# Optimization experiments

Hardware: AMD Instinct MI355X
Metric: run time of the kernel (lower is better)

## Reference

```python
import jax, jax.numpy as jnp
import numpy as np

N = 100000
G = 65          # grid points per axis
C = 16          # channels per receptor grid
IN_FEATS = 16
LIG_F = 128
REC_F = 128
BOTH_F = 128
HID = 256
POCKET_RADIUS = 16.0

# standard uniform cubic B-spline basis matrix (rows: powers 1,t,t^2,t^3)
BSPLINE_M = np.array([[1., 4., 1., 0.],
                      [-3., 0., 3., 0.],
                      [3., -6., 3., 0.],
                      [-1., 3., -3., 1.]], dtype=np.float32) / 6.0


def _spline_w(t, M):
    # t: [N] fractional coords -> [N,4] B-spline weights
    p = jnp.stack([jnp.ones_like(t), t, t * t, t * t * t], axis=-1)  # [N,4]
    return p @ M


def interpolate_grid_3d(grid, pos_norm):
    """grid: [G,G,G,C], pos_norm: [N,3] in [0,1] -> [N,C]."""
    M = jnp.asarray(BSPLINE_M)
    g = grid.shape[0]
    u = pos_norm * (g - 1)                      # [N,3] grid coords
    i0 = jnp.floor(u).astype(jnp.int32)
    t = u - i0                                  # fractional part [N,3]
    offs = jnp.arange(-1, 3, dtype=jnp.int32)   # 4-point stencil
    idx = jnp.clip(i0[:, :, None] + offs[None, None, :], 0, g - 1)  # [N,3,4]
    wx = _spline_w(t[:, 0], M)                  # [N,4]
    wy = _spline_w(t[:, 1], M)
    wz = _spline_w(t[:, 2], M)
    # gather 4x4x4 neighborhood: [N,4,4,4,C]
    vals = grid[idx[:, 0, :, None, None], idx[:, 1, None, :, None], idx[:, 2, None, None, :]]
    return jnp.einsum('nijkc,ni,nj,nk->nc', vals, wx, wy, wz)


def setup_inputs() -> dict:
    key = jax.random.key(0)
    ks = jax.random.split(key, 16)
    s = 0.02
    return {
        'pos': jax.random.uniform(ks[0], (N, 3), jnp.float32, -POCKET_RADIUS, POCKET_RADIUS),
        'nb_params': jax.random.normal(ks[1], (N, IN_FEATS), jnp.float32),
        'batch': jnp.sort(jax.random.randint(ks[2], (N,), 0, 64)),
        'rec_grid0': jax.random.normal(ks[3], (G, G, G, C), jnp.float32) * s,
        'rec_grid1': jax.random.normal(ks[4], (G, G, G, C), jnp.float32) * s,
        'lig_W': jax.random.normal(ks[5], (IN_FEATS, LIG_F), jnp.float32) * s,
        'lig_b': jnp.zeros((LIG_F,), jnp.float32),
        'rec_W': jax.random.normal(ks[6], (2 * C, REC_F), jnp.float32) * s,
        'rec_b': jnp.zeros((REC_F,), jnp.float32),
        'lig_both_W': jax.random.normal(ks[7], (LIG_F, BOTH_F), jnp.float32) * s,
        'lig_both_b': jnp.zeros((BOTH_F,), jnp.float32),
        'rec_both_W': jax.random.normal(ks[8], (REC_F, BOTH_F), jnp.float32) * s,
        'rec_both_b': jnp.zeros((BOTH_F,), jnp.float32),
        'final_W': jax.random.normal(ks[9], (LIG_F + REC_F + BOTH_F, HID), jnp.float32) * s,
        'final_b': jnp.zeros((HID,), jnp.float32),
    }


def reference(pos, nb_params, batch, rec_grid0, rec_grid1, lig_W, lig_b,
              rec_W, rec_b, lig_both_W, lig_both_b, rec_both_W, rec_both_b,
              final_W, final_b):
    # poc_center = 0, pocket_radius = POCKET_RADIUS
    pos_norm = jnp.clip(0.5 + 0.5 * (pos / POCKET_RADIUS), 0.0, 1.0)
    rec_x = jnp.concatenate([interpolate_grid_3d(rec_grid0, pos_norm),
                             interpolate_grid_3d(rec_grid1, pos_norm)], axis=-1)
    rec_x = rec_x @ rec_W + rec_b                      # [N,REC_F] (dropout=identity, eval)
    lig_x = nb_params @ lig_W + lig_b                  # [N,LIG_F]
    lig_both = lig_x @ lig_both_W + lig_both_b         # [N,BOTH_F]
    rec_both = rec_x @ rec_both_W + rec_both_b
    both_x = lig_both * rec_both                       # gated fusion
    x = jnp.concatenate([lig_x, rec_x, both_x], axis=-1) @ final_W + final_b
    return x  # [N, HID]; downstream GNN (TorchMD_ET/TensorNet) is out of scope
```

## Files before the change

### kernel.cpp

```cpp
#include <hip/hip_runtime.h>

typedef __attribute__((ext_vector_type(8))) short short8;
typedef __attribute__((ext_vector_type(4))) float f32x4;

#define N_PTS    100000
#define N_ROWS_P 100096
#define N_CELLS  274625
#define GB_ELEMS (N_CELLS * 32)

static __device__ __forceinline__ unsigned short f2bf(float f) {
    unsigned int u = __builtin_bit_cast(unsigned int, f);
    u += 0x7fffu + ((u >> 16) & 1u);
    return (unsigned short)(u >> 16);
}
static __device__ __forceinline__ float bflo(unsigned int u) {
    return __builtin_bit_cast(float, u << 16);
}
static __device__ __forceinline__ float bfhi(unsigned int u) {
    return __builtin_bit_cast(float, u & 0xffff0000u);
}
static __device__ __forceinline__ unsigned long long pack4bf(f32x4 v) {
    return (unsigned long long)f2bf(v[0])
         | ((unsigned long long)f2bf(v[1]) << 16)
         | ((unsigned long long)f2bf(v[2]) << 32)
         | ((unsigned long long)f2bf(v[3]) << 48);
}

__global__ __launch_bounds__(256) void prep_grids(
        const float* __restrict__ g0, const float* __restrict__ g1,
        unsigned short* __restrict__ gb) {
    int tid = blockIdx.x * 256 + threadIdx.x;
    if (tid >= N_CELLS * 8) return;
    int chunk = tid & 7, cell = tid >> 3;
    const float* src = (chunk < 4) ? (g0 + (size_t)cell * 16 + chunk * 4)
                                   : (g1 + (size_t)cell * 16 + (chunk - 4) * 4);
    float4 v = *(const float4*)src;
    unsigned long long pk = (unsigned long long)f2bf(v.x)
                          | ((unsigned long long)f2bf(v.y) << 16)
                          | ((unsigned long long)f2bf(v.z) << 32)
                          | ((unsigned long long)f2bf(v.w) << 48);
    *(unsigned long long*)(gb + (size_t)cell * 32 + chunk * 4) = pk;
}

__global__ __launch_bounds__(256) void prep_weights(
        const float* __restrict__ ligW, const float* __restrict__ recW,
        const float* __restrict__ w1, const float* __restrict__ w2,
        const float* __restrict__ wf,
        unsigned short* __restrict__ ligWt, unsigned short* __restrict__ recWt,
        unsigned short* __restrict__ w1t, unsigned short* __restrict__ w2t,
        unsigned short* __restrict__ wft) {
    int tid = blockIdx.x * 256 + threadIdx.x;
    if (tid < 4096) {
        int n = tid >> 5, k = tid & 31;
        ligWt[tid] = (k < 16) ? f2bf(ligW[k * 128 + n]) : (unsigned short)0;
    } else if (tid < 8192) {
        int e = tid - 4096; int n = e >> 5, k = e & 31;
        recWt[e] = f2bf(recW[k * 128 + n]);
    } else if (tid < 24576) {
        int e = tid - 8192; int n = e >> 7, k = e & 127;
        w1t[e] = f2bf(w1[k * 128 + n]);
    } else if (tid < 40960) {
        int e = tid - 24576; int n = e >> 7, k = e & 127;
        w2t[e] = f2bf(w2[k * 128 + n]);
    } else if (tid < 139264) {
        int e = tid - 40960; int n = e / 384, k = e - n * 384;
        wft[e] = f2bf(wf[k * 256 + n]);
    }
}

__global__ __launch_bounds__(256) void interp_kernel(
        const float* __restrict__ pos, const float* __restrict__ nb,
        const unsigned short* __restrict__ gb,
        unsigned short* __restrict__ nbb, unsigned short* __restrict__ reccat) {
    int tid = blockIdx.x * 256 + threadIdx.x;
    int pt = tid >> 2;
    int sub = tid & 3;
    if (pt >= N_PTS) return;

    {
        float4 v = *(const float4*)(nb + (size_t)pt * 16 + sub * 4);
        unsigned long long pk = (unsigned long long)f2bf(v.x)
                              | ((unsigned long long)f2bf(v.y) << 16)
                              | ((unsigned long long)f2bf(v.z) << 32)
                              | ((unsigned long long)f2bf(v.w) << 48);
        *(unsigned long long*)(nbb + (size_t)pt * 16 + sub * 4) = pk;
    }

    float w[3][4]; int jj[3][4];
    #pragma unroll
    for (int a = 0; a < 3; a++) {
        float p = pos[(size_t)pt * 3 + a];
        float pn = fminf(fmaxf(0.5f + p * 0.03125f, 0.0f), 1.0f);
        float u = pn * 64.0f;
        float fl = floorf(u);
        int i0 = (int)fl;
        float t = u - fl;
        float t2 = t * t, t3 = t2 * t;
        w[a][0] = (1.0f - 3.0f*t + 3.0f*t2 - t3) * (1.0f/6.0f);
        w[a][1] = (4.0f - 6.0f*t2 + 3.0f*t3) * (1.0f/6.0f);
        w[a][2] = (1.0f + 3.0f*t + 3.0f*t2 - 3.0f*t3) * (1.0f/6.0f);
        w[a][3] = t3 * (1.0f/6.0f);
        jj[a][0] = max(i0 - 1, 0);
        jj[a][1] = i0;
        jj[a][2] = min(i0 + 1, 64);
        jj[a][3] = min(i0 + 2, 64);
    }

    float wz = w[2][sub];
    int jz = jj[2][sub];

    float acc[32];
    #pragma unroll
    for (int c = 0; c < 32; c++) acc[c] = 0.0f;

    #pragma unroll
    for (int ax = 0; ax < 4; ax++) {
        int xoff = jj[0][ax] * 4225;
        float wx = w[0][ax];
        #pragma unroll
        for (int ay = 0; ay < 4; ay++) {
            float ww = wx * w[1][ay] * wz;
            const uint4* p = (const uint4*)(gb + ((size_t)(xoff + jj[1][ay] * 65 + jz) << 5));
            uint4 q0 = p[0], q1 = p[1], q2 = p[2], q3 = p[3];
            unsigned int vv[16] = {q0.x,q0.y,q0.z,q0.w, q1.x,q1.y,q1.z,q1.w,
                                   q2.x,q2.y,q2.z,q2.w, q3.x,q3.y,q3.z,q3.w};
            #pragma unroll
            for (int h = 0; h < 16; h++) {
                acc[2*h]   = fmaf(ww, bflo(vv[h]), acc[2*h]);
                acc[2*h+1] = fmaf(ww, bfhi(vv[h]), acc[2*h+1]);
            }
        }
    }

    #pragma unroll
    for (int c = 0; c < 32; c++) {
        acc[c] += __shfl_xor(acc[c], 1);
        acc[c] += __shfl_xor(acc[c], 2);
    }

    unsigned int rk[4];
    #pragma unroll
    for (int h = 0; h < 4; h++) {
        int c = sub * 8 + 2 * h;
        rk[h] = (unsigned)f2bf(acc[c]) | ((unsigned)f2bf(acc[c+1]) << 16);
    }
    *(uint4*)(reccat + (size_t)pt * 32 + sub * 8) = make_uint4(rk[0], rk[1], rk[2], rk[3]);
}

#define ACT_ADDR(row, kbyte) ((row) * 768 + ((kbyte) ^ (((row) & 7) << 4)))

__global__ __launch_bounds__(512) void fused_mlp(
        const unsigned short* __restrict__ nbb,
        const unsigned short* __restrict__ reccat,
        const unsigned short* __restrict__ ligWt,
        const unsigned short* __restrict__ recWt,
        const unsigned short* __restrict__ w1t,
        const unsigned short* __restrict__ w2t,
        const unsigned short* __restrict__ wft,
        const float* __restrict__ lig_b, const float* __restrict__ rec_b,
        const float* __restrict__ b1, const float* __restrict__ b2,
        const float* __restrict__ fb, float* __restrict__ out) {
    __shared__ __align__(16) char actB[128 * 768];

    int w = threadIdx.x >> 6, lane = threadIdx.x & 63;
    int r = lane & 15, q = lane >> 4;
    int wm = w >> 2, wn = w & 3;
    int mrow0 = blockIdx.x * 128;
    int nf0 = wn * 32;

    {
        short8 bN[4], bC[4];
        #pragma unroll
        for (int mf = 0; mf < 4; mf++) {
            int row = mrow0 + wm * 64 + mf * 16 + r;
            short8 z = {0,0,0,0,0,0,0,0};
            bN[mf] = (q < 2) ? *(const short8*)(nbb + (size_t)row * 16 + q * 8) : z;
            bC[mf] = *(const short8*)(reccat + (size_t)row * 32 + q * 8);
        }
        #pragma unroll
        for (int nf = 0; nf < 2; nf++) {
            int n = nf0 + nf * 16 + r;
            short8 aWl = *(const short8*)(ligWt + n * 32 + q * 8);
            short8 aWr = *(const short8*)(recWt + n * 32 + q * 8);
            f32x4 bl4 = *(const f32x4*)(lig_b + nf0 + nf * 16 + q * 4);
            f32x4 br4 = *(const f32x4*)(rec_b + nf0 + nf * 16 + q * 4);
            #pragma unroll
            for (int mf = 0; mf < 4; mf++) {
                int row_l = wm * 64 + mf * 16 + r;
                int kb = (nf0 + nf * 16 + q * 4) * 2;
                f32x4 dL = __builtin_amdgcn_mfma_f32_16x16x32_bf16(aWl, bN[mf], bl4, 0, 0, 0);
                f32x4 dR = __builtin_amdgcn_mfma_f32_16x16x32_bf16(aWr, bC[mf], br4, 0, 0, 0);
                *(unsigned long long*)(actB + ACT_ADDR(row_l, kb))       = pack4bf(dL);
                *(unsigned long long*)(actB + ACT_ADDR(row_l, 256 + kb)) = pack4bf(dR);
            }
        }
    }
    __syncthreads();

    {
        #pragma unroll
        for (int nf = 0; nf < 2; nf++) {
            int n = nf0 + nf * 16 + r;
            short8 a1[4], a2[4];
            #pragma unroll
            for (int ks = 0; ks < 4; ks++) {
                a1[ks] = *(const short8*)(w1t + n * 128 + ks * 32 + q * 8);
                a2[ks] = *(const short8*)(w2t + n * 128 + ks * 32 + q * 8);
            }
            f32x4 c1 = *(const f32x4*)(b1 + nf0 + nf * 16 + q * 4);
            f32x4 c2 = *(const f32x4*)(b2 + nf0 + nf * 16 + q * 4);
            #pragma unroll
            for (int mf = 0; mf < 4; mf++) {
                int row_l = wm * 64 + mf * 16 + r;
                f32x4 u1 = c1, u2 = c2;
                #pragma unroll
                for (int ks = 0; ks < 4; ks++) {
                    short8 bl = *(const short8*)(actB + ACT_ADDR(row_l, ks * 64 + q * 16));
                    short8 br = *(const short8*)(actB + ACT_ADDR(row_l, 256 + ks * 64 + q * 16));
                    u1 = __builtin_amdgcn_mfma_f32_16x16x32_bf16(a1[ks], bl, u1, 0, 0, 0);
                    u2 = __builtin_amdgcn_mfma_f32_16x16x32_bf16(a2[ks], br, u2, 0, 0, 0);
                }
                f32x4 pr = u1 * u2;
                int kb = 512 + (nf0 + nf * 16 + q * 4) * 2;
                *(unsigned long long*)(actB + ACT_ADDR(row_l, kb)) = pack4bf(pr);
            }
        }
    }
    __syncthreads();

    {
        f32x4 acc[4][4];
        #pragma unroll
        for (int nf = 0; nf < 4; nf++) {
            f32x4 fb4 = *(const f32x4*)(fb + wn * 64 + nf * 16 + q * 4);
            #pragma unroll
            for (int mf = 0; mf < 4; mf++) acc[mf][nf] = fb4;
        }
        #pragma unroll 4
        for (int ks = 0; ks < 12; ks++) {
            short8 bact[4];
            #pragma unroll
            for (int mf = 0; mf < 4; mf++)
                bact[mf] = *(const short8*)(actB + ACT_ADDR(wm * 64 + mf * 16 + r, ks * 64 + q * 16));
            #pragma unroll
            for (int nf = 0; nf < 4; nf++) {
                int n = wn * 64 + nf * 16 + r;
                short8 aw = *(const short8*)(wft + (size_t)n * 384 + ks * 32 + q * 8);
                #pragma unroll
                for (int mf = 0; mf < 4; mf++)
                    acc[mf][nf] = __builtin_amdgcn_mfma_f32_16x16x32_bf16(aw, bact[mf], acc[mf][nf], 0, 0, 0);
            }
        }
        #pragma unroll
        for (int mf = 0; mf < 4; mf++) {
            int grow = mrow0 + wm * 64 + mf * 16 + r;
            if (grow < N_PTS) {
                float* op = out + (size_t)grow * 256 + wn * 64 + q * 4;
                #pragma unroll
                for (int nf = 0; nf < 4; nf++)
                    *(f32x4*)(op + nf * 16) = acc[mf][nf];
            }
        }
    }
}

extern "C" void kernel_launch(void* const* d_in, const int* in_sizes, int n_in,
                              void* d_out, int out_size, void* d_ws, size_t ws_size,
                              hipStream_t stream) {
    const float* pos   = (const float*)d_in[0];
    const float* nb    = (const float*)d_in[1];
    const float* g0    = (const float*)d_in[3];
    const float* g1    = (const float*)d_in[4];
    const float* ligW  = (const float*)d_in[5];
    const float* lig_b = (const float*)d_in[6];
    const float* recW  = (const float*)d_in[7];
    const float* rec_b = (const float*)d_in[8];
    const float* w1    = (const float*)d_in[9];
    const float* b1    = (const float*)d_in[10];
    const float* w2    = (const float*)d_in[11];
    const float* b2    = (const float*)d_in[12];
    const float* wf    = (const float*)d_in[13];
    const float* fbias = (const float*)d_in[14];
    float* out = (float*)d_out;

    char* ws = (char*)d_ws;
    size_t off = 0;
    auto alloc = [&](size_t bytes) {
        char* p = ws + off;
        off = (off + bytes + 255) & ~(size_t)255;
        return p;
    };
    unsigned short* gb     = (unsigned short*)alloc((size_t)GB_ELEMS * 2);
    unsigned short* nbb    = (unsigned short*)alloc((size_t)N_ROWS_P * 16 * 2);
    unsigned short* reccat = (unsigned short*)alloc((size_t)N_ROWS_P * 32 * 2);
    unsigned short* ligWt  = (unsigned short*)alloc(4096 * 2);
    unsigned short* recWt  = (unsigned short*)alloc(4096 * 2);
    unsigned short* w1t    = (unsigned short*)alloc(16384 * 2);
    unsigned short* w2t    = (unsigned short*)alloc(16384 * 2);
    unsigned short* wft    = (unsigned short*)alloc(98304 * 2);

    hipLaunchKernelGGL(prep_grids, dim3((N_CELLS * 8 + 255) / 256), dim3(256), 0, stream,
                       g0, g1, gb);
    hipLaunchKernelGGL(prep_weights, dim3((139264 + 255) / 256), dim3(256), 0, stream,
                       ligW, recW, w1, w2, wf, ligWt, recWt, w1t, w2t, wft);
    hipLaunchKernelGGL(interp_kernel, dim3((N_PTS * 4 + 255) / 256), dim3(256), 0, stream,
                       pos, nb, gb, nbb, reccat);
    hipLaunchKernelGGL(fused_mlp, dim3(N_ROWS_P / 128), dim3(512), 0, stream,
                       nbb, reccat, ligWt, recWt, w1t, w2t, wft,
                       lig_b, rec_b, b1, b2, fbias, out);
}
```

Measured before the change: 323.7 us.

## Split interp channels across lanes and halve MLP row tile for occupancy

The interpolation kernel now uses 8 threads per point, each covering one z-offset and half of the 32 channels, which halves per-thread accumulators and loads. The fused MLP now processes 64 rows per block instead of 128, shrinking LDS use and fragment registers, with a launch-bounds occupancy hint of 6. The w1/w2 weight fragments are hoisted to the start of the kernel. The aim is more resident waves to hide gather and global-load latency, at the cost of more blocks, more redundant weight loads per output row, and more shuffle traffic.

```diff
diff --git a/kernel.cpp b/kernel.cpp
--- a/kernel.cpp
+++ b/kernel.cpp
@@ -4,7 +4,7 @@
 typedef __attribute__((ext_vector_type(4))) float f32x4;
 
 #define N_PTS    100000
-#define N_ROWS_P 100096
+#define N_ROWS_P 100032
 #define N_CELLS  274625
 #define GB_ELEMS (N_CELLS * 32)
 
@@ -73,17 +73,15 @@
         const unsigned short* __restrict__ gb,
         unsigned short* __restrict__ nbb, unsigned short* __restrict__ reccat) {
     int tid = blockIdx.x * 256 + threadIdx.x;
-    int pt = tid >> 2;
-    int sub = tid & 3;
+    int pt = tid >> 3;
+    int sub = tid & 7;
     if (pt >= N_PTS) return;
+    int az = sub >> 1, half = sub & 1;
 
     {
-        float4 v = *(const float4*)(nb + (size_t)pt * 16 + sub * 4);
-        unsigned long long pk = (unsigned long long)f2bf(v.x)
-                              | ((unsigned long long)f2bf(v.y) << 16)
-                              | ((unsigned long long)f2bf(v.z) << 32)
-                              | ((unsigned long long)f2bf(v.w) << 48);
-        *(unsigned long long*)(nbb + (size_t)pt * 16 + sub * 4) = pk;
+        float2 v = *(const float2*)(nb + (size_t)pt * 16 + sub * 2);
+        unsigned pk = (unsigned)f2bf(v.x) | ((unsigned)f2bf(v.y) << 16);
+        *(unsigned*)(nbb + (size_t)pt * 16 + sub * 2) = pk;
     }
 
     float w[3][4]; int jj[3][4];
@@ -106,12 +104,12 @@
         jj[a][3] = min(i0 + 2, 64);
     }
 
-    float wz = w[2][sub];
-    int jz = jj[2][sub];
-
-    float acc[32];
-    #pragma unroll
-    for (int c = 0; c < 32; c++) acc[c] = 0.0f;
+    float wz = w[2][az];
+    int jz = jj[2][az];
+
+    float acc[16];
+    #pragma unroll
+    for (int c = 0; c < 16; c++) acc[c] = 0.0f;
 
     #pragma unroll
     for (int ax = 0; ax < 4; ax++) {
@@ -120,12 +118,11 @@
         #pragma unroll
         for (int ay = 0; ay < 4; ay++) {
             float ww = wx * w[1][ay] * wz;
-            const uint4* p = (const uint4*)(gb + ((size_t)(xoff + jj[1][ay] * 65 + jz) << 5));
-            uint4 q0 = p[0], q1 = p[1], q2 = p[2], q3 = p[3];
-            unsigned int vv[16] = {q0.x,q0.y,q0.z,q0.w, q1.x,q1.y,q1.z,q1.w,
-                                   q2.x,q2.y,q2.z,q2.w, q3.x,q3.y,q3.z,q3.w};
-            #pragma unroll
-            for (int h = 0; h < 16; h++) {
+            const uint4* p = (const uint4*)(gb + ((size_t)(xoff + jj[1][ay] * 65 + jz) << 5) + half * 16);
+            uint4 q0 = p[0], q1 = p[1];
+            unsigned int vv[8] = {q0.x,q0.y,q0.z,q0.w, q1.x,q1.y,q1.z,q1.w};
+            #pragma unroll
+            for (int h = 0; h < 8; h++) {
                 acc[2*h]   = fmaf(ww, bflo(vv[h]), acc[2*h]);
                 acc[2*h+1] = fmaf(ww, bfhi(vv[h]), acc[2*h+1]);
             }
@@ -133,23 +130,25 @@
     }
 
     #pragma unroll
-    for (int c = 0; c < 32; c++) {
-        acc[c] += __shfl_xor(acc[c], 1);
+    for (int c = 0; c < 16; c++) {
         acc[c] += __shfl_xor(acc[c], 2);
-    }
-
-    unsigned int rk[4];
-    #pragma unroll
-    for (int h = 0; h < 4; h++) {
-        int c = sub * 8 + 2 * h;
-        rk[h] = (unsigned)f2bf(acc[c]) | ((unsigned)f2bf(acc[c+1]) << 16);
-    }
-    *(uint4*)(reccat + (size_t)pt * 32 + sub * 8) = make_uint4(rk[0], rk[1], rk[2], rk[3]);
+        acc[c] += __shfl_xor(acc[c], 4);
+    }
+
+    if (az == 0) {
+        unsigned rk[8];
+        #pragma unroll
+        for (int h = 0; h < 8; h++)
+            rk[h] = (unsigned)f2bf(acc[2*h]) | ((unsigned)f2bf(acc[2*h+1]) << 16);
+        uint4* rdst = (uint4*)(reccat + (size_t)pt * 32 + half * 16);
+        rdst[0] = make_uint4(rk[0], rk[1], rk[2], rk[3]);
+        rdst[1] = make_uint4(rk[4], rk[5], rk[6], rk[7]);
+    }
 }
 
 #define ACT_ADDR(row, kbyte) ((row) * 768 + ((kbyte) ^ (((row) & 7) << 4)))
 
-__global__ __launch_bounds__(512) void fused_mlp(
+__global__ __launch_bounds__(512, 6) void fused_mlp(
         const unsigned short* __restrict__ nbb,
         const unsigned short* __restrict__ reccat,
         const unsigned short* __restrict__ ligWt,
@@ -160,19 +159,30 @@
         const float* __restrict__ lig_b, const float* __restrict__ rec_b,
         const float* __restrict__ b1, const float* __restrict__ b2,
         const float* __restrict__ fb, float* __restrict__ out) {
-    __shared__ __align__(16) char actB[128 * 768];
+    __shared__ __align__(16) char actB[64 * 768];
 
     int w = threadIdx.x >> 6, lane = threadIdx.x & 63;
     int r = lane & 15, q = lane >> 4;
     int wm = w >> 2, wn = w & 3;
-    int mrow0 = blockIdx.x * 128;
+    int mrow0 = blockIdx.x * 64;
     int nf0 = wn * 32;
 
+    short8 a1[2][4], a2[2][4];
+    #pragma unroll
+    for (int nf = 0; nf < 2; nf++) {
+        int n = nf0 + nf * 16 + r;
+        #pragma unroll
+        for (int ks = 0; ks < 4; ks++) {
+            a1[nf][ks] = *(const short8*)(w1t + n * 128 + ks * 32 + q * 8);
+            a2[nf][ks] = *(const short8*)(w2t + n * 128 + ks * 32 + q * 8);
+        }
+    }
+
     {
-        short8 bN[4], bC[4];
-        #pragma unroll
-        for (int mf = 0; mf < 4; mf++) {
-            int row = mrow0 + wm * 64 + mf * 16 + r;
+        short8 bN[2], bC[2];
+        #pragma unroll
+        for (int mf = 0; mf < 2; mf++) {
+            int row = mrow0 + wm * 32 + mf * 16 + r;
             short8 z = {0,0,0,0,0,0,0,0};
             bN[mf] = (q < 2) ? *(const short8*)(nbb + (size_t)row * 16 + q * 8) : z;
             bC[mf] = *(const short8*)(reccat + (size_t)row * 32 + q * 8);
@@ -185,8 +195,8 @@
             f32x4 bl4 = *(const f32x4*)(lig_b + nf0 + nf * 16 + q * 4);
             f32x4 br4 = *(const f32x4*)(rec_b + nf0 + nf * 16 + q * 4);
             #pragma unroll
-            for (int mf = 0; mf < 4; mf++) {
-                int row_l = wm * 64 + mf * 16 + r;
+            for (int mf = 0; mf < 2; mf++) {
+                int row_l = wm * 32 + mf * 16 + r;
                 int kb = (nf0 + nf * 16 + q * 4) * 2;
                 f32x4 dL = __builtin_amdgcn_mfma_f32_16x16x32_bf16(aWl, bN[mf], bl4, 0, 0, 0);
                 f32x4 dR = __builtin_amdgcn_mfma_f32_16x16x32_bf16(aWr, bC[mf], br4, 0, 0, 0);
@@ -200,25 +210,18 @@
     {
         #pragma unroll
         for (int nf = 0; nf < 2; nf++) {
-            int n = nf0 + nf * 16 + r;
-            short8 a1[4], a2[4];
-            #pragma unroll
-            for (int ks = 0; ks < 4; ks++) {
-                a1[ks] = *(const short8*)(w1t + n * 128 + ks * 32 + q * 8);
-                a2[ks] = *(const short8*)(w2t + n * 128 + ks * 32 + q * 8);
-            }
             f32x4 c1 = *(const f32x4*)(b1 + nf0 + nf * 16 + q * 4);
             f32x4 c2 = *(const f32x4*)(b2 + nf0 + nf * 16 + q * 4);
             #pragma unroll
-            for (int mf = 0; mf < 4; mf++) {
-                int row_l = wm * 64 + mf * 16 + r;
+            for (int mf = 0; mf < 2; mf++) {
+                int row_l = wm * 32 + mf * 16 + r;
                 f32x4 u1 = c1, u2 = c2;
                 #pragma unroll
                 for (int ks = 0; ks < 4; ks++) {
                     short8 bl = *(const short8*)(actB + ACT_ADDR(row_l, ks * 64 + q * 16));
                     short8 br = *(const short8*)(actB + ACT_ADDR(row_l, 256 + ks * 64 + q * 16));
-                    u1 = __builtin_amdgcn_mfma_f32_16x16x32_bf16(a1[ks], bl, u1, 0, 0, 0);
-                    u2 = __builtin_amdgcn_mfma_f32_16x16x32_bf16(a2[ks], br, u2, 0, 0, 0);
+                    u1 = __builtin_amdgcn_mfma_f32_16x16x32_bf16(a1[nf][ks], bl, u1, 0, 0, 0);
+                    u2 = __builtin_amdgcn_mfma_f32_16x16x32_bf16(a2[nf][ks], br, u2, 0, 0, 0);
                 }
                 f32x4 pr = u1 * u2;
                 int kb = 512 + (nf0 + nf * 16 + q * 4) * 2;
@@ -229,31 +232,31 @@
     __syncthreads();
 
     {
-        f32x4 acc[4][4];
+        f32x4 acc[2][4];
         #pragma unroll
         for (int nf = 0; nf < 4; nf++) {
             f32x4 fb4 = *(const f32x4*)(fb + wn * 64 + nf * 16 + q * 4);
             #pragma unroll
-            for (int mf = 0; mf < 4; mf++) acc[mf][nf] = fb4;
+            for (int mf = 0; mf < 2; mf++) acc[mf][nf] = fb4;
         }
         #pragma unroll 4
         for (int ks = 0; ks < 12; ks++) {
-            short8 bact[4];
-            #pragma unroll
-            for (int mf = 0; mf < 4; mf++)
-                bact[mf] = *(const short8*)(actB + ACT_ADDR(wm * 64 + mf * 16 + r, ks * 64 + q * 16));
+            short8 bact[2];
+            #pragma unroll
+            for (int mf = 0; mf < 2; mf++)
+                bact[mf] = *(const short8*)(actB + ACT_ADDR(wm * 32 + mf * 16 + r, ks * 64 + q * 16));
             #pragma unroll
             for (int nf = 0; nf < 4; nf++) {
                 int n = wn * 64 + nf * 16 + r;
                 short8 aw = *(const short8*)(wft + (size_t)n * 384 + ks * 32 + q * 8);
                 #pragma unroll
-                for (int mf = 0; mf < 4; mf++)
+                for (int mf = 0; mf < 2; mf++)
                     acc[mf][nf] = __builtin_amdgcn_mfma_f32_16x16x32_bf16(aw, bact[mf], acc[mf][nf], 0, 0, 0);
             }
         }
         #pragma unroll
-        for (int mf = 0; mf < 4; mf++) {
-            int grow = mrow0 + wm * 64 + mf * 16 + r;
+        for (int mf = 0; mf < 2; mf++) {
+            int grow = mrow0 + wm * 32 + mf * 16 + r;
             if (grow < N_PTS) {
                 float* op = out + (size_t)grow * 256 + wn * 64 + q * 4;
                 #pragma unroll
@@ -303,9 +306,9 @@
                        g0, g1, gb);
     hipLaunchKernelGGL(prep_weights, dim3((139264 + 255) / 256), dim3(256), 0, stream,
                        ligW, recW, w1, w2, wf, ligWt, recWt, w1t, w2t, wft);
-    hipLaunchKernelGGL(interp_kernel, dim3((N_PTS * 4 + 255) / 256), dim3(256), 0, stream,
+    hipLaunchKernelGGL(interp_kernel, dim3((N_PTS * 8 + 255) / 256), dim3(256), 0, stream,
                        pos, nb, gb, nbb, reccat);
-    hipLaunchKernelGGL(fused_mlp, dim3(N_ROWS_P / 128), dim3(512), 0, stream,
+    hipLaunchKernelGGL(fused_mlp, dim3(N_ROWS_P / 64), dim3(512), 0, stream,
                        nbb, reccat, ligWt, recWt, w1t, w2t, wft,
                        lig_b, rec_b, b1, b2, fbias, out);
 }
```

Result: slower. 397.3 us (+22.7%).
